# Optimization experiments

Hardware: AMD Instinct MI355X
Metric: run time of the kernel (lower is better)

The kernel has to match this reference:

```python
import jax, jax.numpy as jnp
import numpy as np

N = 50000      # nodes
E = 800000     # edges
D_IN = 128
D_H = 512
D_OUT = 256
G = 512        # graphs in batch
EPS_GIN = 0.0  # GINConv default eps
LRELU_SLOPE = 1.5


def setup_inputs() -> dict:
    key = jax.random.key(0)
    ks = jax.random.split(key, 16)
    x = jax.random.normal(ks[0], (N, D_IN), dtype=jnp.float32)
    edge_index = jax.random.randint(ks[1], (2, E), 0, N, dtype=jnp.int64)
    batch = jnp.sort(jax.random.randint(ks[2], (N,), 0, G, dtype=jnp.int64))
    def lin(k, fan_in, fan_out):
        bound = 1.0 / np.sqrt(fan_in)
        k1, k2 = jax.random.split(k)
        W = jax.random.uniform(k1, (fan_in, fan_out), jnp.float32, -bound, bound)
        b = jax.random.uniform(k2, (fan_out,), jnp.float32, -bound, bound)
        return W, b
    W1, b1 = lin(ks[3], D_IN, D_H)
    W2, b2 = lin(ks[4], D_H, D_H)
    W3, b3 = lin(ks[5], D_H, D_H)
    W4, b4 = lin(ks[6], D_H, D_H)
    Wl, bl = lin(ks[7], D_H, D_OUT)
    return {"x": x, "edge_index": edge_index, "batch": batch,
            "W1": W1, "b1": b1, "W2": W2, "b2": b2,
            "W3": W3, "b3": b3, "W4": W4, "b4": b4,
            "Wl": Wl, "bl": bl}


def reference(x, edge_index, batch, W1, b1, W2, b2, W3, b3, W4, b4, Wl, bl):
    # GIN aggregation: sum neighbor (source) features at each target node
    src, dst = edge_index[0], edge_index[1]
    agg = jax.ops.segment_sum(x[src], dst, num_segments=N)  # [N, D_IN]
    h = (1.0 + EPS_GIN) * x + agg
    # 4-layer MLP (Dropout inactive in eval; LeakyReLU negative_slope=1.5)
    h = h @ W1 + b1
    h = jnp.where(h > 0, h, LRELU_SLOPE * h)
    h = jax.nn.relu(h @ W2 + b2)
    h = jax.nn.relu(h @ W3 + b3)
    h = h @ W4 + b4                      # [N, D_H]
    # global mean pool over graphs
    sums = jax.ops.segment_sum(h, batch, num_segments=G)          # [G, D_H]
    cnt = jax.ops.segment_sum(jnp.ones((N, 1), h.dtype), batch, num_segments=G)
    pooled = sums / jnp.maximum(cnt, 1.0)
    out = pooled @ Wl + bl               # [G, D_OUT]
    # F.normalize(dim=1, eps=1e-12)
    nrm = jnp.linalg.norm(out, axis=1, keepdims=True)
    return out / jnp.maximum(nrm, 1e-12)
```

## Files before the change

kernel.cpp:

```cpp
#include <hip/hip_runtime.h>
#include <hip/hip_bf16.h>
#include <cstdint>
#include <cstddef>

#define N_NODES 50000
#define N_EDGES 800000
#define D_IN 128
#define D_H 512
#define D_OUT 256
#define N_GRAPHS 512

#define BM 128
#define BN 256
#define BK 32
#define NBLK ((N_NODES + 255) / 256)
#define CT_SW 264
#define N_MT 391
#define MT_PER_XCD 49

#define NBUCK 196
#define BCAP 6144
#define E_PER_BLK 4096

#define SCAT_BLKS 196
#define TR_BLKS 240
#define CVTX_BLKS ((N_NODES * D_IN / 2 + 64 + 255) / 256)
#define MID_BLKS (SCAT_BLKS + TR_BLKS + CVTX_BLKS)

#define PSLOTS 5

#define XQ_SCALE 4096.0f
#define XQ_INV (1.0f / 4096.0f)

typedef __bf16 v8bf __attribute__((ext_vector_type(8)));
typedef float v4f __attribute__((ext_vector_type(4)));
typedef int v4i __attribute__((ext_vector_type(4)));

__device__ __forceinline__ float bf2f(unsigned short b) {
  return __uint_as_float(((unsigned int)b) << 16);
}
__device__ __forceinline__ unsigned short f2bf(float f) {
  unsigned int u = __float_as_uint(f);
  u += 0x7FFFu + ((u >> 16) & 1u);
  return (unsigned short)(u >> 16);
}

__device__ __forceinline__ void gload_lds16(const void* g, void* l) {
  __builtin_amdgcn_global_load_lds(
      (const __attribute__((address_space(1))) void*)g,
      (__attribute__((address_space(3))) void*)l, 16, 0, 0);
}

__global__ __launch_bounds__(256) void k_prep(const void* __restrict__ x,
                                              const void* __restrict__ ei,
                                              const void* __restrict__ batch,
                                              int* __restrict__ gcur,
                                              int* __restrict__ flags) {
  __shared__ int cnt[3];
  int t = threadIdx.x;
  gcur[t] = 0;
  if (t < 3) cnt[t] = 0;
  __syncthreads();
  const unsigned short* xs = (const unsigned short*)x;
  int c0 = 0;
  for (int k = t; k < 4096; k += 256) {
    unsigned int e = (xs[k] >> 7) & 0xFFu;
    if (e >= 0x90u) c0++;
  }
  atomicAdd(&cnt[0], c0);
  const int* e32 = (const int*)ei;
  int c1 = 0;
  for (int k = t; k < 512; k += 256)
    if (e32[2 * k + 1] != 0) c1++;
  atomicAdd(&cnt[1], c1);
  const int* b32 = (const int*)batch;
  int c2 = 0;
  {
    int w = (N_NODES - 512) + 2 * t + 1;
    if (b32[w] != 0) c2++;
  }
  atomicAdd(&cnt[2], c2);
  __syncthreads();
  if (t == 0) {
    flags[0] = (cnt[0] > 16) ? 1 : 0;
    flags[1] = (cnt[1] == 0) ? 1 : 0;
    flags[2] = (cnt[2] == 0) ? 1 : 0;
  }
}

__global__ __launch_bounds__(256) void k_mid(
    const void* __restrict__ x, const int* __restrict__ ei,
    const int* __restrict__ flags,
    const void* W1, const void* W2, const void* W3, const void* W4,
    const void* Wl, unsigned short* W1T, unsigned short* W2T,
    unsigned short* W3T, unsigned short* W4T, unsigned short* WlT,
    int* __restrict__ gcur, unsigned int* __restrict__ pairs,
    unsigned int* __restrict__ xi, int ne) {
  __shared__ __align__(16) char mshm[20480];
  int bid = blockIdx.x;
  int t = threadIdx.x;

  if (bid < SCAT_BLKS) {
    int* hist = (int*)mshm;
    int* sstart = hist + 256;
    int* gbase = sstart + 256;
    int* sh = gbase + 256;
    unsigned int* lbuf = (unsigned int*)(mshm + 4096);
    int e0 = bid * E_PER_BLK;
    int nloc = ne - e0;
    if (nloc > E_PER_BLK) nloc = E_PER_BLK;
    hist[t] = 0;
    __syncthreads();
    bool fe64 = flags[1] != 0;
    unsigned int pk[16];
    short bk[16], rk[16];
#pragma unroll
    for (int it = 0; it < 16; ++it) {
      int li = it * 256 + t;
      bk[it] = -1;
      if (li < nloc) {
        size_t e = (size_t)e0 + li;
        int s = fe64 ? ei[2 * e] : ei[e];
        int d = fe64 ? ei[2 * ((size_t)ne + e)] : ei[(size_t)ne + e];
        int b = d >> 8;
        pk[it] = (unsigned int)(s & 0xFFFF) | ((unsigned int)(d & 255) << 16) |
                 ((unsigned int)b << 24);
        bk[it] = (short)b;
        rk[it] = (short)atomicAdd(&hist[b], 1);
      }
    }
    __syncthreads();
    int cnt = hist[t];
    sh[t] = cnt;
    __syncthreads();
    for (int o = 1; o < 256; o <<= 1) {
      int a = sh[t];
      int bb = (t >= o) ? sh[t - o] : 0;
      __syncthreads();
      sh[t] = a + bb;
      __syncthreads();
    }
    sstart[t] = sh[t] - cnt;
    gbase[t] = (cnt > 0) ? atomicAdd(&gcur[t], cnt) : 0;
    __syncthreads();
#pragma unroll
    for (int it = 0; it < 16; ++it)
      if (bk[it] >= 0) lbuf[sstart[bk[it]] + rk[it]] = pk[it];
    __syncthreads();
    for (int i = t; i < nloc; i += 256) {
      unsigned int v = lbuf[i];
      int b = v >> 24;
      int off = gbase[b] + (i - sstart[b]);
      if (off < BCAP) pairs[(size_t)b * BCAP + off] = v;
    }
    return;
  }

  if (bid < SCAT_BLKS + TR_BLKS) {
    typedef unsigned short row65[65];
    row65* tile = (row65*)mshm;
    int b2 = bid - SCAT_BLKS;
    const void* src;
    unsigned short* dst;
    int R, C, tb;
    if (b2 < 16)        { src = W1; dst = W1T; R = 128; C = 512; tb = b2; }
    else if (b2 < 80)   { src = W2; dst = W2T; R = 512; C = 512; tb = b2 - 16; }
    else if (b2 < 144)  { src = W3; dst = W3T; R = 512; C = 512; tb = b2 - 80; }
    else if (b2 < 208)  { src = W4; dst = W4T; R = 512; C = 512; tb = b2 - 144; }
    else                { src = Wl; dst = WlT; R = 512; C = 256; tb = b2 - 208; }
    int tpr = C >> 6;
    int r0 = (tb / tpr) << 6, c0 = (tb % tpr) << 6;
    bool f32 = flags[0] != 0;
#pragma unroll
    for (int k = 0; k < 16; ++k) {
      int idx = k * 256 + t;
      int r = idx >> 6, c = idx & 63;
      unsigned short v =
          f32 ? f2bf(((const float*)src)[(size_t)(r0 + r) * C + c0 + c])
              : ((const unsigned short*)src)[(size_t)(r0 + r) * C + c0 + c];
      tile[c][r] = v;
    }
    __syncthreads();
#pragma unroll
    for (int k = 0; k < 16; ++k) {
      int idx = k * 256 + t;
      int r = idx >> 6, c = idx & 63;
      dst[(size_t)(c0 + r) * R + r0 + c] = tile[r][c];
    }
    return;
  }

  int i = (bid - SCAT_BLKS - TR_BLKS) * 256 + t;
  if (i >= N_NODES * D_IN / 2) {
    if (i < N_NODES * D_IN / 2 + 64) xi[i] = 0;
    return;
  }
  float v0, v1;
  if (flags[0]) {
    const float* xf = (const float*)x + (size_t)i * 2;
    v0 = xf[0];
    v1 = xf[1];
  } else {
    unsigned int p = ((const unsigned int*)x)[i];
    v0 = __uint_as_float((p & 0xFFFFu) << 16);
    v1 = __uint_as_float(p & 0xFFFF0000u);
  }
  int q0 = __float2int_rn(fminf(fmaxf(v0, -7.99f), 7.99f) * XQ_SCALE);
  int q1 = __float2int_rn(fminf(fmaxf(v1, -7.99f), 7.99f) * XQ_SCALE);
  xi[i] = ((unsigned int)q0 & 0xFFFFu) | ((unsigned int)q1 << 16);
}

__global__ __launch_bounds__(256) void kb_sort(
    const unsigned int* __restrict__ pairs, const int* __restrict__ gcur,
    int* __restrict__ rowptr, unsigned short* __restrict__ elist) {
  __shared__ int sh[256];
  __shared__ int cursor[256];
  __shared__ unsigned int lpair[BCAP];
  __shared__ unsigned short sorted[BCAP];
  int b = blockIdx.x, t = threadIdx.x;
  int c = (t < NBUCK) ? gcur[t] : 0;
  if (c > BCAP) c = BCAP;
  sh[t] = c;
  __syncthreads();
  for (int o = 1; o < 256; o <<= 1) {
    int a = sh[t];
    int v = (t >= o) ? sh[t - o] : 0;
    __syncthreads();
    sh[t] = a + v;
    __syncthreads();
  }
  int base = (b == 0) ? 0 : sh[b - 1];
  int cnt = sh[b] - base;
  cursor[t] = 0;
  __syncthreads();
  for (int i = t; i < cnt; i += 256) {
    unsigned int v = pairs[(size_t)b * BCAP + i];
    lpair[i] = v;
    atomicAdd(&cursor[(v >> 16) & 255], 1);
  }
  __syncthreads();
  int nc = cursor[t];
  sh[t] = nc;
  __syncthreads();
  for (int o = 1; o < 256; o <<= 1) {
    int a = sh[t];
    int v = (t >= o) ? sh[t - o] : 0;
    __syncthreads();
    sh[t] = a + v;
    __syncthreads();
  }
  int nstart = sh[t] - nc;
  cursor[t] = nstart;
  int node = b * 256 + t;
  if (node <= N_NODES) rowptr[node] = base + nstart;
  __syncthreads();
  for (int i = t; i < cnt; i += 256) {
    unsigned int v = lpair[i];
    int r = atomicAdd(&cursor[(v >> 16) & 255], 1);
    sorted[r] = (unsigned short)(v & 0xFFFFu);
  }
  __syncthreads();
  for (int i = t; i < cnt; i += 256)
    elist[base + i] = sorted[i];
}

__global__ __launch_bounds__(256) void k_gather(
    const unsigned int* __restrict__ xi, const int* __restrict__ rowptr,
    const unsigned short* __restrict__ elist, unsigned int* __restrict__ h0) {
  int node = blockIdx.x * 4 + (threadIdx.x >> 6);
  if (node >= N_NODES) return;
  int lane = threadIdx.x & 63;
  int l15 = lane & 15;
  int grp = lane >> 4;
  int s0 = rowptr[node], s1 = rowptr[node + 1];
  int a[8];
  {
    v4i self = (v4i){0, 0, 0, 0};
    if (lane < 16) self = *(const v4i*)(xi + (size_t)node * 64 + l15 * 4);
#pragma unroll
    for (int q = 0; q < 4; ++q) {
      a[2 * q]     = (int)(short)(self[q] & 0xFFFF);
      a[2 * q + 1] = self[q] >> 16;
    }
  }
  for (int j0 = s0; j0 < s1; j0 += 64) {
    int jj = j0 + lane;
    int cnt = s1 - j0;
    cnt = cnt < 64 ? cnt : 64;
    int ev = (jj < s1) ? (int)elist[jj] : N_NODES;
    for (int j = 0; j < cnt; j += 4) {
      int src = __shfl(ev, j + grp, 64);
      v4i p = *(const v4i*)(xi + (size_t)src * 64 + l15 * 4);
#pragma unroll
      for (int q = 0; q < 4; ++q) {
        a[2 * q]     += (int)(short)(p[q] & 0xFFFF);
        a[2 * q + 1] += p[q] >> 16;
      }
    }
  }
#pragma unroll
  for (int k = 0; k < 8; ++k) {
    a[k] += __shfl_xor(a[k], 16, 64);
    a[k] += __shfl_xor(a[k], 32, 64);
  }
  if (lane < 16) {
    v4i o;
#pragma unroll
    for (int q = 0; q < 4; ++q) {
      unsigned int lo = f2bf((float)a[2 * q] * XQ_INV);
      unsigned int hi = f2bf((float)a[2 * q + 1] * XQ_INV);
      o[q] = (int)(lo | (hi << 16));
    }
    *(v4i*)(h0 + (size_t)node * 64 + l15 * 4) = o;
  }
}

template <int ACT, int OUT, bool SWZ>
__global__ __launch_bounds__(512, 4) void gemm_bt(
    const unsigned short* __restrict__ A,
    const unsigned short* __restrict__ BT,
    const void* __restrict__ bias, const int* __restrict__ flags,
    const int* __restrict__ batchp, void* __restrict__ Cout,
    int M, int K, int Nc) {
  __shared__ __align__(16) unsigned short smem[2][BM * BK + BN * BK];

  const int tid  = threadIdx.x;
  const int wave = tid >> 6;
  const int lane = tid & 63;
  const int quad = lane >> 4;
  const int l15  = lane & 15;
  int m0, n0;
  if (SWZ) {
    int xcd = blockIdx.x & 7;
    int l = blockIdx.x >> 3;
    int mt = xcd * MT_PER_XCD + (l >> 1);
    if (mt >= N_MT) return;
    m0 = mt * BM;
    n0 = (l & 1) * BN;
  } else {
    n0 = blockIdx.x * BN;
    m0 = blockIdx.y * BM;
  }
  const int wm = (wave >> 2) * 64;
  const int wn = (wave & 3) * 64;
  const bool fm = flags[0] != 0;

  v4f acc[4][4];
#pragma unroll
  for (int i = 0; i < 4; ++i)
#pragma unroll
    for (int j = 0; j < 4; ++j) acc[i][j] = (v4f){0.f, 0.f, 0.f, 0.f};

  auto stage = [&](int kt, int buf) {
    const int k0 = kt * BK;
    unsigned short* As = smem[buf];
    unsigned short* Bs = smem[buf] + BM * BK;
    {
      int L = tid;
      int row = L >> 2;
      int c = (L & 3) ^ ((row >> 1) & 3);
      int gr = m0 + row;
      gr = gr < M ? gr : (M - 1);
      gload_lds16(A + (size_t)gr * K + (k0 + c * 8), As + (size_t)L * 8);
    }
#pragma unroll
    for (int it = 0; it < 2; ++it) {
      int L = tid + it * 512;
      int row = L >> 2;
      int c = (L & 3) ^ ((row >> 1) & 3);
      int gn = n0 + row;
      gload_lds16(BT + (size_t)gn * K + (k0 + c * 8), Bs + (size_t)L * 8);
    }
  };

  const int nK = K / BK;
  stage(0, 0);
  for (int kt = 0; kt < nK; ++kt) {
    __syncthreads();
    if (kt + 1 < nK) stage(kt + 1, (kt + 1) & 1);
    const unsigned short* As = smem[kt & 1];
    const unsigned short* Bs = smem[kt & 1] + BM * BK;
    v8bf af[4], bfr[4];
#pragma unroll
    for (int mi = 0; mi < 4; ++mi) {
      int r = wm + mi * 16 + l15;
      int s = quad ^ ((r >> 1) & 3);
      af[mi] = *(const v8bf*)(As + (r * 4 + s) * 8);
    }
#pragma unroll
    for (int ni = 0; ni < 4; ++ni) {
      int r = wn + ni * 16 + l15;
      int s = quad ^ ((r >> 1) & 3);
      bfr[ni] = *(const v8bf*)(Bs + (r * 4 + s) * 8);
    }
#pragma unroll
    for (int mi = 0; mi < 4; ++mi)
#pragma unroll
      for (int ni = 0; ni < 4; ++ni)
        acc[mi][ni] = __builtin_amdgcn_mfma_f32_16x16x32_bf16(
            af[mi], bfr[ni], acc[mi][ni], 0, 0, 0);
  }

  float bv[4];
#pragma unroll
  for (int ni = 0; ni < 4; ++ni) {
    int col = n0 + wn + ni * 16 + l15;
    bv[ni] = fm ? ((const float*)bias)[col]
                : bf2f(((const unsigned short*)bias)[col]);
  }
#pragma unroll
  for (int mi = 0; mi < 4; ++mi)
#pragma unroll
    for (int ni = 0; ni < 4; ++ni)
#pragma unroll
      for (int rg = 0; rg < 4; ++rg) {
        float v = acc[mi][ni][rg] + bv[ni];
        if (ACT == 0) v = v > 0.f ? v : 1.5f * v;
        if (ACT == 1) v = v > 0.f ? v : 0.f;
        acc[mi][ni][rg] = v;
      }

  if (OUT == 1) {
#pragma unroll
    for (int ni = 0; ni < 4; ++ni) {
      int col = n0 + wn + ni * 16 + l15;
#pragma unroll
      for (int mi = 0; mi < 4; ++mi)
#pragma unroll
        for (int rg = 0; rg < 4; ++rg) {
          int row = m0 + wm + mi * 16 + quad * 4 + rg;
          if (row < M)
            ((float*)Cout)[(size_t)row * Nc + col] = acc[mi][ni][rg];
        }
    }
    return;
  }

  if (OUT == 2) {
    float* ssq = (float*)smem;
    __syncthreads();
    float pp[4][4];
#pragma unroll
    for (int mi = 0; mi < 4; ++mi)
#pragma unroll
      for (int rg = 0; rg < 4; ++rg) {
        float s = 0.f;
#pragma unroll
        for (int ni = 0; ni < 4; ++ni) {
          float v = acc[mi][ni][rg];
          s += v * v;
        }
#pragma unroll
        for (int o = 1; o < 16; o <<= 1) s += __shfl_xor(s, o, 64);
        pp[mi][rg] = s;
      }
    if (l15 == 0) {
#pragma unroll
      for (int mi = 0; mi < 4; ++mi)
#pragma unroll
        for (int rg = 0; rg < 4; ++rg)
          ssq[(wave & 3) * 128 + wm + mi * 16 + quad * 4 + rg] = pp[mi][rg];
    }
    __syncthreads();
#pragma unroll
    for (int mi = 0; mi < 4; ++mi)
#pragma unroll
      for (int rg = 0; rg < 4; ++rg) {
        int row = wm + mi * 16 + quad * 4 + rg;
        float tot = (ssq[row] + ssq[128 + row]) + (ssq[256 + row] + ssq[384 + row]);
        float inv = 1.0f / fmaxf(sqrtf(tot), 1e-12f);
        int grow = m0 + row;
#pragma unroll
        for (int ni = 0; ni < 4; ++ni) {
          int col = wn + ni * 16 + l15;
          float r = acc[mi][ni][rg] * inv;
          if (fm)
            ((float*)Cout)[(size_t)grow * Nc + col] = r;
          else
            ((unsigned short*)Cout)[(size_t)grow * Nc + col] = f2bf(r);
        }
      }
    return;
  }

  if (OUT == 3) {
    float* part = (float*)smem;
    __syncthreads();
    for (int i = tid; i < 8 * PSLOTS * 256; i += 512) part[i] = 0.f;
    const int contrib = (wave >> 2) * 4 + quad;
    const bool b64 = flags[2] != 0;
    int g0 = b64 ? batchp[2 * (size_t)m0] : batchp[m0];
    __syncthreads();
    int curslot = -1;
    float r0 = 0.f, r1 = 0.f, r2 = 0.f, r3 = 0.f;
#pragma unroll
    for (int mi = 0; mi < 4; ++mi)
#pragma unroll
      for (int rg = 0; rg < 4; ++rg) {
        int grow = m0 + wm + mi * 16 + quad * 4 + rg;
        if (grow < M) {
          int gv = (b64 ? batchp[2 * (size_t)grow] : batchp[grow]) - g0;
          gv = gv < 0 ? 0 : (gv >= PSLOTS ? PSLOTS - 1 : gv);
          if (gv != curslot) {
            if (curslot >= 0) {
              float* pp = part + (contrib * PSLOTS + curslot) * 256 + wn + l15;
              pp[0] += r0; pp[16] += r1; pp[32] += r2; pp[48] += r3;
            }
            curslot = gv;
            r0 = r1 = r2 = r3 = 0.f;
          }
          r0 += acc[mi][0][rg];
          r1 += acc[mi][1][rg];
          r2 += acc[mi][2][rg];
          r3 += acc[mi][3][rg];
        }
      }
    if (curslot >= 0) {
      float* pp = part + (contrib * PSLOTS + curslot) * 256 + wn + l15;
      pp[0] += r0; pp[16] += r1; pp[32] += r2; pp[48] += r3;
    }
    __syncthreads();
    float* pb = (float*)Cout;
    int mt = m0 >> 7;
    int nh = n0 >> 8;
    size_t base = (size_t)(mt * 2 + nh) * (PSLOTS * 256);
    for (int i = tid; i < PSLOTS * 256; i += 512) {
      float s = ((part[i] + part[1 * PSLOTS * 256 + i]) +
                 (part[2 * PSLOTS * 256 + i] + part[3 * PSLOTS * 256 + i])) +
                ((part[4 * PSLOTS * 256 + i] + part[5 * PSLOTS * 256 + i]) +
                 (part[6 * PSLOTS * 256 + i] + part[7 * PSLOTS * 256 + i]));
      pb[base + i] = s;
    }
    return;
  }

  unsigned short* Ct = (unsigned short*)smem;
  __syncthreads();
#pragma unroll
  for (int h = 0; h < 2; ++h) {
    if ((wave >> 2) == h) {
#pragma unroll
      for (int mi = 0; mi < 4; ++mi)
#pragma unroll
        for (int ni = 0; ni < 4; ++ni)
#pragma unroll
          for (int rg = 0; rg < 4; ++rg) {
            int lr = mi * 16 + quad * 4 + rg;
            int c = wn + ni * 16 + l15;
            Ct[lr * CT_SW + c] = f2bf(acc[mi][ni][rg]);
          }
    }
    __syncthreads();
    int rl0 = tid >> 5;
    int ch = tid & 31;
#pragma unroll
    for (int p = 0; p < 4; ++p) {
      int rl = rl0 + p * 16;
      int grow = m0 + h * 64 + rl;
      if (grow < M) {
        v4i val = *(const v4i*)(Ct + rl * CT_SW + ch * 8);
        *(v4i*)((unsigned short*)Cout + (size_t)grow * Nc + n0 + ch * 8) = val;
      }
    }
    __syncthreads();
  }
}

__global__ __launch_bounds__(256) void k_cvtpool(
    const float* __restrict__ pb, const int* __restrict__ batch,
    const int* __restrict__ flags, unsigned int* __restrict__ pooled) {
  __shared__ int bounds[2];
  int g = blockIdx.x, t = threadIdx.x;
  bool b64 = flags[2] != 0;
  if (t < 2) {
    int key = g + t;
    int lo = 0, hi = N_NODES;
    while (lo < hi) {
      int mid = (lo + hi) >> 1;
      int bv = b64 ? batch[2 * (size_t)mid] : batch[mid];
      if (bv < key) lo = mid + 1; else hi = mid;
    }
    bounds[t] = lo;
  }
  __syncthreads();
  int s0 = bounds[0], s1 = bounds[1];
  int c0 = 2 * t;
  int nh = c0 >> 8;
  int cl = c0 & 255;
  float a0 = 0.f, a1 = 0.f;
  if (s1 > s0) {
    int mtlo = s0 >> 7, mthi = (s1 - 1) >> 7;
    for (int mt = mtlo; mt <= mthi; ++mt) {
      int g0 = b64 ? batch[2 * (size_t)(mt * 128)] : batch[mt * 128];
      int slot = g - g0;
      if (slot >= 0 && slot < PSLOTS) {
        size_t base = (size_t)(mt * 2 + nh) * (PSLOTS * 256) + (size_t)slot * 256;
        a0 += pb[base + cl];
        a1 += pb[base + cl + 1];
      }
    }
  }
  float inv = 1.0f / fmaxf((float)(s1 - s0), 1.0f);
  unsigned int lo2 = f2bf(a0 * inv);
  unsigned int hi2 = f2bf(a1 * inv);
  pooled[(size_t)g * (D_H / 2) + t] = lo2 | (hi2 << 16);
}

extern "C" void kernel_launch(void* const* d_in, const int* in_sizes, int n_in,
                              void* d_out, int out_size, void* d_ws,
                              size_t ws_size, hipStream_t stream) {
  const void* x    = d_in[0];
  const int* ei    = (const int*)d_in[1];
  const int* batch = (const int*)d_in[2];
  const void* W1 = d_in[3];
  const void* b1 = d_in[4];
  const void* W2 = d_in[5];
  const void* b2 = d_in[6];
  const void* W3 = d_in[7];
  const void* b3 = d_in[8];
  const void* W4 = d_in[9];
  const void* b4 = d_in[10];
  const void* Wl = d_in[11];
  const void* bl = d_in[12];

  char* ws = (char*)d_ws;
  size_t off = 0;
  auto alloc = [&](size_t bytes) {
    void* p = ws + off;
    off += (bytes + 255) & ~(size_t)255;
    return p;
  };
  int* flags           = (int*)alloc(64);
  unsigned short* W1T  = (unsigned short*)alloc((size_t)D_IN * D_H * 2);
  unsigned short* W2T  = (unsigned short*)alloc((size_t)D_H * D_H * 2);
  unsigned short* W3T  = (unsigned short*)alloc((size_t)D_H * D_H * 2);
  unsigned short* W4T  = (unsigned short*)alloc((size_t)D_H * D_H * 2);
  unsigned short* WlT  = (unsigned short*)alloc((size_t)D_H * D_OUT * 2);
  unsigned int* pooled3 = (unsigned int*)alloc((size_t)N_GRAPHS * D_H * 2);
  unsigned int* pooled4 = (unsigned int*)alloc((size_t)N_GRAPHS * D_H * 2);
  float* pb            = (float*)alloc((size_t)N_MT * 2 * PSLOTS * 256 * 4);
  int* gcur   = (int*)alloc(256 * 4);
  int* rowptr = (int*)alloc(((size_t)N_NODES + 1) * 4);
  unsigned short* elist = (unsigned short*)alloc((size_t)N_EDGES * 2);
  void* S1 = alloc((size_t)N_NODES * D_H * 2);
  void* S2 = alloc((size_t)N_NODES * D_H * 2);
  unsigned int* xi   = (unsigned int*)S1;
  unsigned short* hA = (unsigned short*)S1;
  unsigned int* pairs = (unsigned int*)((char*)S1 + ((size_t)16 << 20));
  unsigned int* h0u  = (unsigned int*)S2;
  unsigned short* h0 = (unsigned short*)S2;
  unsigned short* hB = (unsigned short*)S2;

  k_prep<<<1, 256, 0, stream>>>(x, ei, batch, gcur, flags);

  k_mid<<<MID_BLKS, 256, 0, stream>>>(
      x, ei, flags, W1, W2, W3, W4, Wl, W1T, W2T, W3T, W4T, WlT,
      gcur, pairs, xi, N_EDGES);

  kb_sort<<<NBUCK, 256, 0, stream>>>(pairs, gcur, rowptr, elist);
  k_gather<<<(N_NODES + 3) / 4, 256, 0, stream>>>(xi, rowptr, elist, h0u);

  const int gBig = 8 * MT_PER_XCD * 2;
  gemm_bt<0, 0, true><<<gBig, 512, 0, stream>>>(h0, W1T, b1, flags, batch, hA, N_NODES, D_IN, D_H);
  gemm_bt<1, 0, true><<<gBig, 512, 0, stream>>>(hA, W2T, b2, flags, batch, hB, N_NODES, D_H, D_H);
  gemm_bt<1, 3, true><<<gBig, 512, 0, stream>>>(hB, W3T, b3, flags, batch, pb, N_NODES, D_H, D_H);

  k_cvtpool<<<N_GRAPHS, 256, 0, stream>>>(pb, batch, flags, pooled3);

  dim3 g4(D_H / BN, N_GRAPHS / BM);
  gemm_bt<2, 0, false><<<g4, 512, 0, stream>>>(
      (const unsigned short*)pooled3, W4T, b4, flags, batch, pooled4, N_GRAPHS, D_H, D_H);

  dim3 g5(D_OUT / BN, N_GRAPHS / BM);
  gemm_bt<2, 2, false><<<g5, 512, 0, stream>>>(
      (const unsigned short*)pooled4, WlT, bl, flags, batch, d_out, N_GRAPHS, D_H, D_OUT);
}
```

Baseline: 295.3 us.

## Fold W4 and Wl into one combined weight and fuse pooling into final GEMM

Because the final two layers are linear after pooling, the code precomputes a combined weight W4·Wl and bias b4·Wl+bl inside spare blocks of the sort kernel. The last GEMM then loads the pooled partial sums itself and runs once with the combined weight. This removes the separate pooling kernel and one small GEMM launch. The trade-offs are an extra bf16 rounding of the combined weight, and the pooling work now runs in only four blocks, each writing and then reading back its own rows of a pooled buffer.

```diff
diff --git a/kernel.cpp b/kernel.cpp
--- a/kernel.cpp
+++ b/kernel.cpp
@@ -26,6 +26,8 @@
 #define TR_BLKS 240
 #define CVTX_BLKS ((N_NODES * D_IN / 2 + 64 + 255) / 256)
 #define MID_BLKS (SCAT_BLKS + TR_BLKS + CVTX_BLKS)
+
+#define WC_BLKS 64
 
 #define PSLOTS 5
 
@@ -212,12 +214,60 @@
 
 __global__ __launch_bounds__(256) void kb_sort(
     const unsigned int* __restrict__ pairs, const int* __restrict__ gcur,
-    int* __restrict__ rowptr, unsigned short* __restrict__ elist) {
+    int* __restrict__ rowptr, unsigned short* __restrict__ elist,
+    const unsigned short* __restrict__ W4T,
+    const unsigned short* __restrict__ WlT,
+    const void* __restrict__ b4, const void* __restrict__ bl,
+    const int* __restrict__ flags,
+    unsigned short* __restrict__ WcT, float* __restrict__ bc) {
   __shared__ int sh[256];
   __shared__ int cursor[256];
   __shared__ unsigned int lpair[BCAP];
   __shared__ unsigned short sorted[BCAP];
   int b = blockIdx.x, t = threadIdx.x;
+
+  if (b >= NBUCK) {
+    int wb = b - NBUCK;
+    if (wb < WC_BLKS) {
+      float (*wlt)[4] = (float(*)[4])lpair;
+      int n0w = wb * 4;
+      for (int e = t; e < 2048; e += 256) {
+        int j = e >> 2, ns = e & 3;
+        wlt[j][ns] = bf2f(WlT[(size_t)(n0w + ns) * 512 + j]);
+      }
+      __syncthreads();
+      float a0[4] = {0.f, 0.f, 0.f, 0.f}, a1[4] = {0.f, 0.f, 0.f, 0.f};
+      for (int j = 0; j < 512; ++j) {
+        v4f wv = *(const v4f*)&wlt[j][0];
+        float x0 = bf2f(W4T[(size_t)j * 512 + t]);
+        float x1 = bf2f(W4T[(size_t)j * 512 + t + 256]);
+#pragma unroll
+        for (int q = 0; q < 4; ++q) {
+          a0[q] += x0 * wv[q];
+          a1[q] += x1 * wv[q];
+        }
+      }
+#pragma unroll
+      for (int q = 0; q < 4; ++q) {
+        WcT[(size_t)(n0w + q) * 512 + t]       = f2bf(a0[q]);
+        WcT[(size_t)(n0w + q) * 512 + t + 256] = f2bf(a1[q]);
+      }
+    } else {
+      float* bsh = (float*)lpair;
+      bool fmw = flags[0] != 0;
+      for (int e = t; e < 512; e += 256)
+        bsh[e] = fmw ? ((const float*)b4)[e]
+                     : bf2f(((const unsigned short*)b4)[e]);
+      __syncthreads();
+      float a = fmw ? ((const float*)bl)[t]
+                    : bf2f(((const unsigned short*)bl)[t]);
+      for (int j = 0; j < 512; ++j)
+        a += bsh[j] * bf2f(WlT[(size_t)t * 512 + j]);
+      bc[t] = a;
+    }
+    return;
+  }
+
   int c = (t < NBUCK) ? gcur[t] : 0;
   if (c > BCAP) c = BCAP;
   sh[t] = c;
@@ -320,7 +370,8 @@
     const unsigned short* __restrict__ A,
     const unsigned short* __restrict__ BT,
     const void* __restrict__ bias, const int* __restrict__ flags,
-    const int* __restrict__ batchp, void* __restrict__ Cout,
+    const int* __restrict__ batchp, const float* __restrict__ pbin,
+    unsigned short* __restrict__ apool, void* __restrict__ Cout,
     int M, int K, int Nc) {
   __shared__ __align__(16) unsigned short smem[2][BM * BK + BN * BK];
 
@@ -345,6 +396,49 @@
   const int wn = (wave & 3) * 64;
   const bool fm = flags[0] != 0;
 
+  if (OUT == 4) {
+    int* gb = (int*)smem;
+    bool b64b = flags[2] != 0;
+    for (int key = tid; key <= 128; key += 512) {
+      int kk = m0 + key;
+      int lo = 0, hi = N_NODES;
+      while (lo < hi) {
+        int mid = (lo + hi) >> 1;
+        int bv = b64b ? batchp[2 * (size_t)mid] : batchp[mid];
+        if (bv < kk) lo = mid + 1; else hi = mid;
+      }
+      gb[key] = lo;
+    }
+    __syncthreads();
+    int r = tid >> 2;
+    int gg = m0 + r;
+    int s0 = gb[r], s1 = gb[r + 1];
+    float inv = 1.0f / fmaxf((float)(s1 - s0), 1.0f);
+    size_t baseA[3][2];
+    int cnt = 0;
+    if (s1 > s0) {
+      int mtlo = s0 >> 7, mthi = (s1 - 1) >> 7;
+      for (int mt = mtlo; mt <= mthi && cnt < 3; ++mt) {
+        int g0 = b64b ? batchp[2 * (size_t)(mt * 128)] : batchp[mt * 128];
+        int slot = gg - g0;
+        if (slot >= 0 && slot < PSLOTS) {
+          baseA[cnt][0] = (size_t)(mt * 2 + 0) * (PSLOTS * 256) + (size_t)slot * 256;
+          baseA[cnt][1] = (size_t)(mt * 2 + 1) * (PSLOTS * 256) + (size_t)slot * 256;
+          ++cnt;
+        }
+      }
+    }
+    int cbase = (tid & 3) * 128;
+    for (int i = 0; i < 128; ++i) {
+      int cc = cbase + i;
+      int nh = cc >> 8, cl = cc & 255;
+      float a = 0.f;
+      for (int q = 0; q < cnt; ++q) a += pbin[baseA[q][nh] + cl];
+      apool[(size_t)gg * 512 + cc] = f2bf(a * inv);
+    }
+    __syncthreads();
+  }
+
   v4f acc[4][4];
 #pragma unroll
   for (int i = 0; i < 4; ++i)
@@ -405,8 +499,8 @@
 #pragma unroll
   for (int ni = 0; ni < 4; ++ni) {
     int col = n0 + wn + ni * 16 + l15;
-    bv[ni] = fm ? ((const float*)bias)[col]
-                : bf2f(((const unsigned short*)bias)[col]);
+    bv[ni] = (fm || OUT == 4) ? ((const float*)bias)[col]
+                              : bf2f(((const unsigned short*)bias)[col]);
   }
 #pragma unroll
   for (int mi = 0; mi < 4; ++mi)
@@ -436,7 +530,7 @@
     return;
   }
 
-  if (OUT == 2) {
+  if (OUT == 2 || OUT == 4) {
     float* ssq = (float*)smem;
     __syncthreads();
     float pp[4][4];
@@ -566,46 +660,6 @@
   }
 }
 
-__global__ __launch_bounds__(256) void k_cvtpool(
-    const float* __restrict__ pb, const int* __restrict__ batch,
-    const int* __restrict__ flags, unsigned int* __restrict__ pooled) {
-  __shared__ int bounds[2];
-  int g = blockIdx.x, t = threadIdx.x;
-  bool b64 = flags[2] != 0;
-  if (t < 2) {
-    int key = g + t;
-    int lo = 0, hi = N_NODES;
-    while (lo < hi) {
-      int mid = (lo + hi) >> 1;
-      int bv = b64 ? batch[2 * (size_t)mid] : batch[mid];
-      if (bv < key) lo = mid + 1; else hi = mid;
-    }
-    bounds[t] = lo;
-  }
-  __syncthreads();
-  int s0 = bounds[0], s1 = bounds[1];
-  int c0 = 2 * t;
-  int nh = c0 >> 8;
-  int cl = c0 & 255;
-  float a0 = 0.f, a1 = 0.f;
-  if (s1 > s0) {
-    int mtlo = s0 >> 7, mthi = (s1 - 1) >> 7;
-    for (int mt = mtlo; mt <= mthi; ++mt) {
-      int g0 = b64 ? batch[2 * (size_t)(mt * 128)] : batch[mt * 128];
-      int slot = g - g0;
-      if (slot >= 0 && slot < PSLOTS) {
-        size_t base = (size_t)(mt * 2 + nh) * (PSLOTS * 256) + (size_t)slot * 256;
-        a0 += pb[base + cl];
-        a1 += pb[base + cl + 1];
-      }
-    }
-  }
-  float inv = 1.0f / fmaxf((float)(s1 - s0), 1.0f);
-  unsigned int lo2 = f2bf(a0 * inv);
-  unsigned int hi2 = f2bf(a1 * inv);
-  pooled[(size_t)g * (D_H / 2) + t] = lo2 | (hi2 << 16);
-}
-
 extern "C" void kernel_launch(void* const* d_in, const int* in_sizes, int n_in,
                               void* d_out, int out_size, void* d_ws,
                               size_t ws_size, hipStream_t stream) {
@@ -636,8 +690,9 @@
   unsigned short* W3T  = (unsigned short*)alloc((size_t)D_H * D_H * 2);
   unsigned short* W4T  = (unsigned short*)alloc((size_t)D_H * D_H * 2);
   unsigned short* WlT  = (unsigned short*)alloc((size_t)D_H * D_OUT * 2);
-  unsigned int* pooled3 = (unsigned int*)alloc((size_t)N_GRAPHS * D_H * 2);
-  unsigned int* pooled4 = (unsigned int*)alloc((size_t)N_GRAPHS * D_H * 2);
+  unsigned short* WcT  = (unsigned short*)alloc((size_t)D_OUT * D_H * 2);
+  float* bc            = (float*)alloc((size_t)D_OUT * 4);
+  unsigned short* pooled3s = (unsigned short*)alloc((size_t)N_GRAPHS * D_H * 2);
   float* pb            = (float*)alloc((size_t)N_MT * 2 * PSLOTS * 256 * 4);
   int* gcur   = (int*)alloc(256 * 4);
   int* rowptr = (int*)alloc(((size_t)N_NODES + 1) * 4);
@@ -657,21 +712,20 @@
       x, ei, flags, W1, W2, W3, W4, Wl, W1T, W2T, W3T, W4T, WlT,
       gcur, pairs, xi, N_EDGES);
 
-  kb_sort<<<NBUCK, 256, 0, stream>>>(pairs, gcur, rowptr, elist);
+  kb_sort<<<NBUCK + WC_BLKS + 1, 256, 0, stream>>>(
+      pairs, gcur, rowptr, elist, W4T, WlT, b4, bl, flags, WcT, bc);
   k_gather<<<(N_NODES + 3) / 4, 256, 0, stream>>>(xi, rowptr, elist, h0u);
 
   const int gBig = 8 * MT_PER_XCD * 2;
-  gemm_bt<0, 0, true><<<gBig, 512, 0, stream>>>(h0, W1T, b1, flags, batch, hA, N_NODES, D_IN, D_H);
-  gemm_bt<1, 0, true><<<gBig, 512, 0, stream>>>(hA, W2T, b2, flags, batch, hB, N_NODES, D_H, D_H);
-  gemm_bt<1, 3, true><<<gBig, 512, 0, stream>>>(hB, W3T, b3, flags, batch, pb, N_NODES, D_H, D_H);
-
-  k_cvtpool<<<N_GRAPHS, 256, 0, stream>>>(pb, batch, flags, pooled3);
-
-  dim3 g4(D_H / BN, N_GRAPHS / BM);
-  gemm_bt<2, 0, false><<<g4, 512, 0, stream>>>(
-      (const unsigned short*)pooled3, W4T, b4, flags, batch, pooled4, N_GRAPHS, D_H, D_H);
-
-  dim3 g5(D_OUT / BN, N_GRAPHS / BM);
-  gemm_bt<2, 2, false><<<g5, 512, 0, stream>>>(
-      (const unsigned short*)pooled4, WlT, bl, flags, batch, d_out, N_GRAPHS, D_H, D_OUT);
-}
+  gemm_bt<0, 0, true><<<gBig, 512, 0, stream>>>(
+      h0, W1T, b1, flags, batch, nullptr, nullptr, hA, N_NODES, D_IN, D_H);
+  gemm_bt<1, 0, true><<<gBig, 512, 0, stream>>>(
+      hA, W2T, b2, flags, batch, nullptr, nullptr, hB, N_NODES, D_H, D_H);
+  gemm_bt<1, 3, true><<<gBig, 512, 0, stream>>>(
+      hB, W3T, b3, flags, batch, nullptr, nullptr, pb, N_NODES, D_H, D_H);
+
+  dim3 g5(1, 4);
+  gemm_bt<2, 4, false><<<g5, 512, 0, stream>>>(
+      pooled3s, WcT, bc, flags, batch, pb, pooled3s, d_out,
+      N_GRAPHS, D_H, D_OUT);
+}
```

Result: slower. 422.8 us (+43.2%).
